# Kernel optimization log

Measured on AMD Instinct MI355X. Metric: run time of the kernel, lower is better.

Reference implementation:

```python
import jax, jax.numpy as jnp
import numpy as np

H, DH = 16, 64          # num_heads, dim_head
DIM = 1024              # dim_ltn
EPS = 1e-5


def setup_inputs() -> dict:
    key = jax.random.key(0)
    ks = jax.random.split(key, 8)
    b, n_txt, t, m = 2, 2048, 4, 256
    text = jax.random.normal(ks[0], (b, n_txt, DIM), dtype=jnp.float32)
    image = jax.random.normal(ks[1], (b, t, m, DIM), dtype=jnp.float32)
    locations = jax.random.randint(ks[2], (b, n_txt), 0, 2)  # 0/1 media markers
    s = DIM ** -0.5
    Wq = jax.random.normal(ks[3], (DIM, H * DH), dtype=jnp.float32) * s
    Wkv = jax.random.normal(ks[4], (DIM, 2 * H * DH), dtype=jnp.float32) * s
    Wo = jax.random.normal(ks[5], (H * DH, DIM), dtype=jnp.float32) * s
    ln_gamma = jnp.ones((DIM,), dtype=jnp.float32)
    ln_beta = jnp.zeros((DIM,), dtype=jnp.float32)
    return {"text": text, "image": image, "locations": locations,
            "Wq": Wq, "Wkv": Wkv, "Wo": Wo,
            "ln_gamma": ln_gamma, "ln_beta": ln_beta}


def reference(text, image, locations, Wq, Wkv, Wo, ln_gamma, ln_beta):
    scale = DH ** -0.5
    b, t, m, d = image.shape
    # LayerNorm(text)
    mu = text.mean(-1, keepdims=True)
    var = ((text - mu) ** 2).mean(-1, keepdims=True)
    tn = (text - mu) / jnp.sqrt(var + EPS) * ln_gamma + ln_beta
    img = image.reshape(b, t * m, d)             # b (t m) d
    q = tn @ Wq                                  # b n (h dh)
    k, v = jnp.split(img @ Wkv, 2, axis=-1)      # each b tm (h dh)
    split_heads = lambda x: x.reshape(x.shape[0], x.shape[1], H, DH).transpose(0, 2, 1, 3)
    q, k, v = split_heads(q), split_heads(k), split_heads(v)
    attn = jnp.einsum('bhid,bhjd->bhij', q, k) * scale   # b h n (t m)
    txt_time = jnp.cumsum(locations, axis=-1)            # b n : media index per text token
    viz_time = jnp.repeat(jnp.arange(1, t + 1), m)       # (t m)
    # only_attend_to_immediate -> equality mask
    mask = txt_time[:, None, :, None] == viz_time[None, None, None, :]
    neg = -jnp.finfo(attn.dtype).max
    attn = jnp.where(mask, attn, neg)
    attn = jax.nn.softmax(attn, axis=-1)
    # zero attention for text tokens before any media (txt_time == 0)
    attn = jnp.where((txt_time == 0)[:, None, :, None], 0.0, attn)
    out = jnp.einsum('bhij,bhjd->bhid', attn, v)
    out = out.transpose(0, 2, 1, 3).reshape(b, -1, H * DH)
    return out @ Wo
```

## Files before the change

### kernel.cpp

```cpp
#include <hip/hip_runtime.h>

#define BATCH 2
#define NTXT  2048
#define TMED  4
#define MMED  256
#define TM    (TMED * MMED)
#define DIM   1024
#define NH    16
#define DHD   64
#define KVW   2048
#define RMAX  256
#define RT    32
#define QSTR  ((size_t)BATCH * RMAX * DIM)

typedef _Float16 f16x8 __attribute__((ext_vector_type(8)));
typedef float    f32x4 __attribute__((ext_vector_type(4)));

__global__ __launch_bounds__(1024) void k1_scan_ibar(
    const int* __restrict__ loc, const float* __restrict__ image,
    int* __restrict__ tt, int* __restrict__ seg, float* __restrict__ ibar) {
  __shared__ int buf[NTXT];
  __shared__ int s_start, s_end;
  const int idx = blockIdx.x;
  const int tid = threadIdx.x;
  if (idx < BATCH) {
    const int b = idx;
    if (tid == 0) { s_start = NTXT; s_end = NTXT; }
    buf[tid]        = loc[b * NTXT + tid];
    buf[tid + 1024] = loc[b * NTXT + tid + 1024];
    __syncthreads();
    for (int off = 1; off < NTXT; off <<= 1) {
      int a0 = (tid >= off) ? buf[tid - off] : 0;
      int a1 = buf[tid + 1024 - off];
      __syncthreads();
      buf[tid] += a0;
      buf[tid + 1024] += a1;
      __syncthreads();
    }
    const int v0 = buf[tid], v1 = buf[tid + 1024];
    tt[b * NTXT + tid]        = v0;
    tt[b * NTXT + tid + 1024] = v1;
    if (v0 >= 1) atomicMin(&s_start, tid);
    if (v0 >= 5) atomicMin(&s_end, tid);
    if (v1 >= 1) atomicMin(&s_start, tid + 1024);
    if (v1 >= 5) atomicMin(&s_end, tid + 1024);
    __syncthreads();
    if (tid == 0) {
      seg[b * 2]     = s_start;
      seg[b * 2 + 1] = s_end - s_start;
    }
  } else {
    const int j = idx - BATCH;
    const int b = j >> 6, rt = j & 63;
    const float* p = image + (size_t)(b * TM + rt * 16) * DIM + tid;
    float s = 0.f;
#pragma unroll
    for (int r = 0; r < 16; r++) s += p[(size_t)r * DIM];
    atomicAdd(&ibar[b * DIM + tid], s * (1.0f / (float)TM));
  }
}

__global__ __launch_bounds__(256) void k2_prep(
    const float* __restrict__ Wkv, const float* __restrict__ text,
    const float* __restrict__ gamma, const float* __restrict__ beta,
    const int* __restrict__ seg, const float* __restrict__ ibar,
    _Float16* __restrict__ WkvT, float* __restrict__ tn,
    float* __restrict__ vbar) {
  __shared__ float tile[64][65];
  __shared__ float red[256];
  const int idx = blockIdx.x;
  const int tid = threadIdx.x;
  if (idx < 512) {
    const int k0 = (idx & 15) * 64, n0 = (idx >> 4) * 64;
    const int r = tid >> 4, c4 = (tid & 15) * 4;
#pragma unroll
    for (int i = 0; i < 4; i++) {
      const float4 v = *reinterpret_cast<const float4*>(
          Wkv + (size_t)(k0 + r + i * 16) * KVW + n0 + c4);
      tile[r + i * 16][c4 + 0] = v.x; tile[r + i * 16][c4 + 1] = v.y;
      tile[r + i * 16][c4 + 2] = v.z; tile[r + i * 16][c4 + 3] = v.w;
    }
    __syncthreads();
#pragma unroll
    for (int it = 0; it < 2; it++) {
      const int chunk = it * 256 + tid;
      const int n = chunk >> 3, kc = (chunk & 7) * 8;
      f16x8 h;
#pragma unroll
      for (int j = 0; j < 8; j++) h[j] = (_Float16)tile[kc + j][n];
      *reinterpret_cast<f16x8*>(WkvT + (size_t)(n0 + n) * DIM + k0 + kc) = h;
    }
  } else if (idx < 576) {
    const int j = idx - 512;
    const int b = j >> 5, rt = j & 31;
    const int i0 = seg[b * 2];
    const int cnt = min(seg[b * 2 + 1], RMAX);
    for (int r = rt; r < cnt; r += RT) {
      const float* xrow = text + (size_t)(b * NTXT + i0 + r) * DIM;
      float x[4];
      float s = 0.f;
#pragma unroll
      for (int u = 0; u < 4; u++) { x[u] = xrow[tid + 256 * u]; s += x[u]; }
      red[tid] = s; __syncthreads();
      for (int st = 128; st > 0; st >>= 1) {
        if (tid < st) red[tid] += red[tid + st];
        __syncthreads();
      }
      const float mu = red[0] * (1.0f / DIM); __syncthreads();
      float vs = 0.f;
#pragma unroll
      for (int u = 0; u < 4; u++) { float d = x[u] - mu; vs += d * d; }
      red[tid] = vs; __syncthreads();
      for (int st = 128; st > 0; st >>= 1) {
        if (tid < st) red[tid] += red[tid + st];
        __syncthreads();
      }
      const float rstd = rsqrtf(red[0] * (1.0f / DIM) + 1e-5f); __syncthreads();
      float* trow = tn + (size_t)(b * RMAX + r) * DIM;
#pragma unroll
      for (int u = 0; u < 4; u++) {
        const int c = tid + 256 * u;
        trow[c] = (x[u] - mu) * rstd * gamma[c] + beta[c];
      }
      __syncthreads();
    }
  } else {
    const int j = idx - 576;
    const int b = j >> 5, et = (j >> 3) & 3, cc = j & 7;
    const int e = et * 256 + tid;
    const int c0 = cc * 128;
    if (tid < 128) red[tid] = ibar[b * DIM + c0 + tid];
    __syncthreads();
    float s = 0.f;
    for (int c = 0; c < 128; c++)
      s += red[c] * Wkv[(size_t)(c0 + c) * KVW + DIM + e];
    atomicAdd(&vbar[b * DIM + e], s);
  }
}

__global__ __launch_bounds__(512) void k3_gemm_qproj_obar(
    const float* __restrict__ image, const _Float16* __restrict__ WkvT,
    const float* __restrict__ Wq, const float* __restrict__ Wo,
    const float* __restrict__ tn, const float* __restrict__ vbar,
    const int* __restrict__ seg, _Float16* __restrict__ kv16,
    float* __restrict__ qpart, float* __restrict__ obar) {
  __shared__ char smem[24576];
  const int idx = blockIdx.x;
  const int tid = threadIdx.x;
  if (idx < 256) {
    _Float16* As = (_Float16*)smem;
    _Float16* Bs = As + 128 * 32;
    const int lane = tid & 63, wid = tid >> 6;
    const int wm = wid & 3, wn = wid >> 2;
    const int row0 = (idx >> 4) * 128, col0 = (idx & 15) * 128;
    const int srow = tid >> 2, skc = (tid & 3) * 8;
    const int frow = lane & 15, fq = lane >> 4;
    f32x4 acc[2][4] = {};
    for (int k0 = 0; k0 < DIM; k0 += 32) {
      const float* ap = image + (size_t)(row0 + srow) * DIM + k0 + skc;
      const float4 a0 = *reinterpret_cast<const float4*>(ap);
      const float4 a1 = *reinterpret_cast<const float4*>(ap + 4);
      f16x8 av;
      av[0] = (_Float16)a0.x; av[1] = (_Float16)a0.y;
      av[2] = (_Float16)a0.z; av[3] = (_Float16)a0.w;
      av[4] = (_Float16)a1.x; av[5] = (_Float16)a1.y;
      av[6] = (_Float16)a1.z; av[7] = (_Float16)a1.w;
      const f16x8 bv = *reinterpret_cast<const f16x8*>(
          WkvT + (size_t)(col0 + srow) * DIM + k0 + skc);
      __syncthreads();
      *reinterpret_cast<f16x8*>(As + tid * 8) = av;
      *reinterpret_cast<f16x8*>(Bs + tid * 8) = bv;
      __syncthreads();
      f16x8 af[2], bf[4];
#pragma unroll
      for (int mt = 0; mt < 2; mt++)
        af[mt] = *reinterpret_cast<const f16x8*>(
            As + (wm * 32 + mt * 16 + frow) * 32 + fq * 8);
#pragma unroll
      for (int nt = 0; nt < 4; nt++)
        bf[nt] = *reinterpret_cast<const f16x8*>(
            Bs + (wn * 64 + nt * 16 + frow) * 32 + fq * 8);
#pragma unroll
      for (int mt = 0; mt < 2; mt++)
#pragma unroll
        for (int nt = 0; nt < 4; nt++)
          acc[mt][nt] = __builtin_amdgcn_mfma_f32_16x16x32_f16(
              af[mt], bf[nt], acc[mt][nt], 0, 0, 0);
    }
#pragma unroll
    for (int mt = 0; mt < 2; mt++)
#pragma unroll
      for (int nt = 0; nt < 4; nt++) {
        const int col = col0 + wn * 64 + nt * 16 + frow;
#pragma unroll
        for (int r = 0; r < 4; r++) {
          const int row = row0 + wm * 32 + mt * 16 + fq * 4 + r;
          kv16[(size_t)row * KVW + col] = (_Float16)acc[mt][nt][r];
        }
      }
  } else if (idx < 320) {
    float* tn_s = (float*)smem;
    float* qred = tn_s + 8 * 256;
    const int j = idx - 256;
    const int b = j >> 5, nt = (j >> 2) & 7, cc = j & 3;
    const int n0 = nt * 128, c0 = cc * 256;
    const int n = tid & 127, cs = tid >> 7;
    const int cnt = min(seg[b * 2 + 1], RMAX);
    float* qp = qpart + (size_t)cc * QSTR;
    for (int r0 = 0; r0 < cnt; r0 += 8) {
      const int rows = min(8, cnt - r0);
      for (int i = tid; i < 8 * 256; i += 512) {
        const int r = i >> 8, c = i & 255;
        tn_s[i] = (r < rows) ? tn[(size_t)(b * RMAX + r0 + r) * DIM + c0 + c]
                             : 0.f;
      }
      __syncthreads();
      float acc[8] = {};
      for (int ci = 0; ci < 64; ci++) {
        const int c = cs * 64 + ci;
        const float w = Wq[(size_t)(c0 + c) * DIM + n0 + n];
#pragma unroll
        for (int rr = 0; rr < 8; rr++) acc[rr] += tn_s[rr * 256 + c] * w;
      }
#pragma unroll
      for (int rr = 0; rr < 8; rr++) qred[(cs * 8 + rr) * 128 + n] = acc[rr];
      __syncthreads();
      if (cs == 0) {
        for (int rr = 0; rr < rows; rr++) {
          const float s = qred[rr * 128 + n] + qred[(8 + rr) * 128 + n] +
                          qred[(16 + rr) * 128 + n] + qred[(24 + rr) * 128 + n];
          qp[(size_t)(b * RMAX + r0 + rr) * DIM + n0 + n] = s;
        }
      }
      __syncthreads();
    }
  } else {
    float* vb_s = (float*)smem;
    const int j = idx - 320;
    const int b = j >> 4, et = (j >> 3) & 1, cc = j & 7;
    const int e = et * 512 + tid;
    const int c0 = cc * 128;
    if (tid < 128) vb_s[tid] = vbar[b * DIM + c0 + tid];
    __syncthreads();
    float s = 0.f;
    for (int c = 0; c < 128; c++)
      s += vb_s[c] * Wo[(size_t)(c0 + c) * DIM + e];
    atomicAdd(&obar[b * DIM + e], s);
  }
}

__global__ __launch_bounds__(256) void k4_fill_attn(
    const float* __restrict__ text, const _Float16* __restrict__ kv16,
    const float* __restrict__ Wq, const float* __restrict__ Wo,
    const float* __restrict__ gamma, const float* __restrict__ beta,
    const int* __restrict__ tt, const int* __restrict__ seg,
    const float* __restrict__ obar, const float* __restrict__ qpart,
    float* __restrict__ oacc, float* __restrict__ out) {
  __shared__ float red[256];
  __shared__ float pbuf[256];
  const int idx = blockIdx.x;
  const int tid = threadIdx.x;
  if (idx < BATCH * NTXT) {
    const int b = idx >> 11;
    const int i = idx & (NTXT - 1);
    const int t = tt[b * NTXT + i];
    float* orow = out + (size_t)(b * NTXT + i) * DIM;
    if (t == 0) {
      for (int c = tid; c < DIM; c += 256) orow[c] = 0.f;
      return;
    }
    if (t > TMED) {
      const float* ob = obar + b * DIM;
      for (int c = tid; c < DIM; c += 256) orow[c] = ob[c];
      return;
    }
    if (i - seg[b * 2] < RMAX) return;
    __shared__ float tns[DIM];
    __shared__ float qrow[DIM];
    __shared__ float oaccs[DIM];
    const float* xrow = text + (size_t)(b * NTXT + i) * DIM;
    float x[4];
    float s = 0.f;
#pragma unroll
    for (int u = 0; u < 4; u++) { x[u] = xrow[tid + 256 * u]; s += x[u]; }
    red[tid] = s; __syncthreads();
    for (int st = 128; st > 0; st >>= 1) {
      if (tid < st) red[tid] += red[tid + st];
      __syncthreads();
    }
    const float mu = red[0] * (1.0f / DIM); __syncthreads();
    float vs = 0.f;
#pragma unroll
    for (int u = 0; u < 4; u++) { float d = x[u] - mu; vs += d * d; }
    red[tid] = vs; __syncthreads();
    for (int st = 128; st > 0; st >>= 1) {
      if (tid < st) red[tid] += red[tid + st];
      __syncthreads();
    }
    const float rstd = rsqrtf(red[0] * (1.0f / DIM) + 1e-5f); __syncthreads();
#pragma unroll
    for (int u = 0; u < 4; u++) {
      const int c = tid + 256 * u;
      tns[c] = (x[u] - mu) * rstd * gamma[c] + beta[c];
    }
    __syncthreads();
    {
      float qa[4] = {0.f, 0.f, 0.f, 0.f};
      for (int c = 0; c < DIM; c++) {
        const float tv = tns[c];
        const float* w = Wq + (size_t)c * DIM + tid;
#pragma unroll
        for (int u = 0; u < 4; u++) qa[u] += tv * w[256 * u];
      }
#pragma unroll
      for (int u = 0; u < 4; u++) qrow[tid + 256 * u] = qa[u];
    }
    __syncthreads();
    const size_t kvrow0 = (size_t)(b * TM + (t - 1) * MMED) * KVW;
    const int d0 = tid & 63, g = tid >> 6;
    for (int h = 0; h < NH; h++) {
      const _Float16* krow = kv16 + kvrow0 + (size_t)tid * KVW + h * DHD;
      float sc = 0.f;
#pragma unroll
      for (int d = 0; d < DHD; d++) sc += qrow[h * DHD + d] * (float)krow[d];
      sc *= 0.125f;
      red[tid] = sc; __syncthreads();
      for (int st = 128; st > 0; st >>= 1) {
        if (tid < st) red[tid] = fmaxf(red[tid], red[tid + st]);
        __syncthreads();
      }
      const float mx = red[0]; __syncthreads();
      const float e = __expf(sc - mx);
      red[tid] = e; __syncthreads();
      for (int st = 128; st > 0; st >>= 1) {
        if (tid < st) red[tid] += red[tid + st];
        __syncthreads();
      }
      const float inv = 1.0f / red[0]; __syncthreads();
      pbuf[tid] = e * inv; __syncthreads();
      const _Float16* vbase = kv16 + kvrow0 + (size_t)(g * 64) * KVW + DIM + h * DHD + d0;
      float a = 0.f;
#pragma unroll 8
      for (int jj = 0; jj < 64; jj++) a += pbuf[g * 64 + jj] * (float)vbase[(size_t)jj * KVW];
      red[tid] = a; __syncthreads();
      if (tid < 64)
        oaccs[h * DHD + tid] = red[tid] + red[64 + tid] + red[128 + tid] + red[192 + tid];
      __syncthreads();
    }
    float oa[4] = {0.f, 0.f, 0.f, 0.f};
    for (int c = 0; c < DIM; c++) {
      const float ov = oaccs[c];
      const float* w = Wo + (size_t)c * DIM + tid;
#pragma unroll
      for (int u = 0; u < 4; u++) oa[u] += ov * w[256 * u];
    }
#pragma unroll
    for (int u = 0; u < 4; u++) orow[tid + 256 * u] = oa[u];
  } else {
    __shared__ float qs[DHD];
    const int j = idx - BATCH * NTXT;
    const int h = j & 15, rt = (j >> 4) & 31, b = j >> 9;
    const int i0 = seg[b * 2];
    const int cnt = min(seg[b * 2 + 1], RMAX);
    const int d0 = tid & 63, g = tid >> 6;
    for (int r = rt; r < cnt; r += RT) {
      const int i = i0 + r;
      const int t = tt[b * NTXT + i];
      if (tid < 64) {
        const size_t qoff = (size_t)(b * RMAX + r) * DIM + h * DHD + tid;
        qs[tid] = qpart[qoff] + qpart[QSTR + qoff] +
                  qpart[2 * QSTR + qoff] + qpart[3 * QSTR + qoff];
      }
      __syncthreads();
      const size_t kvrow0 = (size_t)(b * TM + (t - 1) * MMED) * KVW;
      const _Float16* krow = kv16 + kvrow0 + (size_t)tid * KVW + h * DHD;
      float sc = 0.f;
#pragma unroll
      for (int d = 0; d < DHD; d += 8) {
        const f16x8 kk = *reinterpret_cast<const f16x8*>(krow + d);
#pragma unroll
        for (int u = 0; u < 8; u++) sc += qs[d + u] * (float)kk[u];
      }
      sc *= 0.125f;
      red[tid] = sc; __syncthreads();
      for (int st = 128; st > 0; st >>= 1) {
        if (tid < st) red[tid] = fmaxf(red[tid], red[tid + st]);
        __syncthreads();
      }
      const float mx = red[0]; __syncthreads();
      const float e = __expf(sc - mx);
      red[tid] = e; __syncthreads();
      for (int st = 128; st > 0; st >>= 1) {
        if (tid < st) red[tid] += red[tid + st];
        __syncthreads();
      }
      const float inv = 1.0f / red[0]; __syncthreads();
      pbuf[tid] = e * inv; __syncthreads();
      const _Float16* vbase = kv16 + kvrow0 + (size_t)(g * 64) * KVW + DIM + h * DHD + d0;
      float a = 0.f;
#pragma unroll 8
      for (int jj = 0; jj < 64; jj++) a += pbuf[g * 64 + jj] * (float)vbase[(size_t)jj * KVW];
      red[tid] = a; __syncthreads();
      if (tid < 64)
        oacc[(size_t)(b * RMAX + r) * DIM + h * DHD + tid] =
            red[tid] + red[64 + tid] + red[128 + tid] + red[192 + tid];
      __syncthreads();
    }
  }
}

__global__ __launch_bounds__(256) void k5_oproj(
    const float* __restrict__ oacc, const float* __restrict__ Wo,
    const int* __restrict__ seg, float* __restrict__ out) {
  const int ct = blockIdx.x;
  const int rt = blockIdx.y;
  const int b = blockIdx.z;
  const int i0 = seg[b * 2];
  const int cnt = min(seg[b * 2 + 1], RMAX);
  const int tid = threadIdx.x;
  const int d0 = tid & 63, g = tid >> 6;
  __shared__ float op[4][64];
  for (int r = rt; r < cnt; r += RT) {
    const float* arow = oacc + (size_t)(b * RMAX + r) * DIM;
    const float* wo = Wo + (size_t)(g * 256) * DIM + ct * 64 + d0;
    float s = 0.f;
    for (int c = 0; c < 256; c++) s += arow[g * 256 + c] * wo[(size_t)c * DIM];
    op[g][d0] = s; __syncthreads();
    if (tid < 64)
      out[(size_t)(b * NTXT + i0 + r) * DIM + ct * 64 + tid] =
          op[0][tid] + op[1][tid] + op[2][tid] + op[3][tid];
    __syncthreads();
  }
}

extern "C" void kernel_launch(void* const* d_in, const int* in_sizes, int n_in,
                              void* d_out, int out_size, void* d_ws, size_t ws_size,
                              hipStream_t stream) {
  const float* text  = (const float*)d_in[0];
  const float* image = (const float*)d_in[1];
  const int*   loc   = (const int*)d_in[2];
  const float* Wq    = (const float*)d_in[3];
  const float* Wkv   = (const float*)d_in[4];
  const float* Wo    = (const float*)d_in[5];
  const float* gamma = (const float*)d_in[6];
  const float* beta  = (const float*)d_in[7];
  float* out = (float*)d_out;

  _Float16* kv16  = (_Float16*)d_ws;
  _Float16* WkvT  = kv16 + (size_t)BATCH * TM * KVW;
  float*    oacc  = (float*)WkvT;
  float*    tn    = (float*)(WkvT + (size_t)KVW * DIM);
  float*    qpart = tn + (size_t)BATCH * RMAX * DIM;
  float*    ibar  = qpart + 4 * QSTR;
  float*    vbar  = ibar + BATCH * DIM;
  float*    obar  = vbar + BATCH * DIM;
  int*      tt    = (int*)(obar + BATCH * DIM);
  int*      seg   = tt + BATCH * NTXT;

  hipMemsetAsync(ibar, 0, 3 * BATCH * DIM * sizeof(float), stream);
  k1_scan_ibar<<<BATCH + 128, 1024, 0, stream>>>(loc, image, tt, seg, ibar);
  k2_prep<<<640, 256, 0, stream>>>(Wkv, text, gamma, beta, seg, ibar,
                                   WkvT, tn, vbar);
  k3_gemm_qproj_obar<<<352, 512, 0, stream>>>(image, WkvT, Wq, Wo, tn, vbar,
                                              seg, kv16, qpart, obar);
  k4_fill_attn<<<BATCH * NTXT + NH * RT * BATCH, 256, 0, stream>>>(
      text, kv16, Wq, Wo, gamma, beta, tt, seg, obar, qpart, oacc, out);
  k5_oproj<<<dim3(16, RT, BATCH), 256, 0, stream>>>(oacc, Wo, seg, out);
}
```

Baseline: 166.3 us.

## Restructure pipeline: fuse LN into q-proj, vbar from GEMM epilogue, fold o-proj into attention

Removes the separate image-mean pass and ibar·Wkv GEMV. vbar is now computed by reducing the V columns of the KV GEMM accumulators in its epilogue. LayerNorm moves into the q-projection blocks using warp-shuffle single-pass statistics, and the prefix scan becomes a per-thread serial scan plus a block scan. The o-projection kernel is dropped: each attention head block multiplies its head output by its slice of Wo and atomically adds into pre-zeroed output rows. This cuts launches and global intermediates, at the cost of many float atomics, nondeterministic summation order and a single-pass variance formula.

```diff
diff --git a/kernel.cpp b/kernel.cpp
--- a/kernel.cpp
+++ b/kernel.cpp
@@ -10,67 +10,53 @@
 #define DHD   64
 #define KVW   2048
 #define RMAX  256
-#define RT    32
 #define QSTR  ((size_t)BATCH * RMAX * DIM)
 
 typedef _Float16 f16x8 __attribute__((ext_vector_type(8)));
 typedef float    f32x4 __attribute__((ext_vector_type(4)));
 
-__global__ __launch_bounds__(1024) void k1_scan_ibar(
-    const int* __restrict__ loc, const float* __restrict__ image,
-    int* __restrict__ tt, int* __restrict__ seg, float* __restrict__ ibar) {
-  __shared__ int buf[NTXT];
+__global__ __launch_bounds__(256) void k1_prep(
+    const int* __restrict__ loc, const float* __restrict__ Wkv,
+    int* __restrict__ tt, int* __restrict__ seg, float* __restrict__ vbar,
+    _Float16* __restrict__ WkvT) {
+  __shared__ float tile[64][65];
+  __shared__ int tots[256];
   __shared__ int s_start, s_end;
-  const int idx = blockIdx.x;
+  const int bid = blockIdx.x;
   const int tid = threadIdx.x;
-  if (idx < BATCH) {
-    const int b = idx;
+  if (bid < BATCH) {
+    const int b = bid;
     if (tid == 0) { s_start = NTXT; s_end = NTXT; }
-    buf[tid]        = loc[b * NTXT + tid];
-    buf[tid + 1024] = loc[b * NTXT + tid + 1024];
-    __syncthreads();
-    for (int off = 1; off < NTXT; off <<= 1) {
-      int a0 = (tid >= off) ? buf[tid - off] : 0;
-      int a1 = buf[tid + 1024 - off];
-      __syncthreads();
-      buf[tid] += a0;
-      buf[tid + 1024] += a1;
-      __syncthreads();
-    }
-    const int v0 = buf[tid], v1 = buf[tid + 1024];
-    tt[b * NTXT + tid]        = v0;
-    tt[b * NTXT + tid + 1024] = v1;
-    if (v0 >= 1) atomicMin(&s_start, tid);
-    if (v0 >= 5) atomicMin(&s_end, tid);
-    if (v1 >= 1) atomicMin(&s_start, tid + 1024);
-    if (v1 >= 5) atomicMin(&s_end, tid + 1024);
+    __syncthreads();
+    int v[8];
+    int run = 0;
+    const int base = b * NTXT + tid * 8;
+#pragma unroll
+    for (int k = 0; k < 8; k++) { run += loc[base + k]; v[k] = run; }
+    tots[tid] = run; __syncthreads();
+    for (int off = 1; off < 256; off <<= 1) {
+      const int add = (tid >= off) ? tots[tid - off] : 0;
+      __syncthreads();
+      tots[tid] += add;
+      __syncthreads();
+    }
+    const int excl = tots[tid] - run;
+#pragma unroll
+    for (int k = 0; k < 8; k++) {
+      const int tv = excl + v[k];
+      tt[base + k] = tv;
+      if (tv >= 1) atomicMin(&s_start, tid * 8 + k);
+      if (tv >= 5) atomicMin(&s_end, tid * 8 + k);
+    }
     __syncthreads();
     if (tid == 0) {
       seg[b * 2]     = s_start;
       seg[b * 2 + 1] = s_end - s_start;
     }
+  } else if (bid == 2) {
+    for (int c = tid; c < 2 * BATCH * DIM; c += 256) vbar[c] = 0.f;
   } else {
-    const int j = idx - BATCH;
-    const int b = j >> 6, rt = j & 63;
-    const float* p = image + (size_t)(b * TM + rt * 16) * DIM + tid;
-    float s = 0.f;
-#pragma unroll
-    for (int r = 0; r < 16; r++) s += p[(size_t)r * DIM];
-    atomicAdd(&ibar[b * DIM + tid], s * (1.0f / (float)TM));
-  }
-}
-
-__global__ __launch_bounds__(256) void k2_prep(
-    const float* __restrict__ Wkv, const float* __restrict__ text,
-    const float* __restrict__ gamma, const float* __restrict__ beta,
-    const int* __restrict__ seg, const float* __restrict__ ibar,
-    _Float16* __restrict__ WkvT, float* __restrict__ tn,
-    float* __restrict__ vbar) {
-  __shared__ float tile[64][65];
-  __shared__ float red[256];
-  const int idx = blockIdx.x;
-  const int tid = threadIdx.x;
-  if (idx < 512) {
+    const int idx = bid - 3;
     const int k0 = (idx & 15) * 64, n0 = (idx >> 4) * 64;
     const int r = tid >> 4, c4 = (tid & 15) * 4;
 #pragma unroll
@@ -90,61 +76,16 @@
       for (int j = 0; j < 8; j++) h[j] = (_Float16)tile[kc + j][n];
       *reinterpret_cast<f16x8*>(WkvT + (size_t)(n0 + n) * DIM + k0 + kc) = h;
     }
-  } else if (idx < 576) {
-    const int j = idx - 512;
-    const int b = j >> 5, rt = j & 31;
-    const int i0 = seg[b * 2];
-    const int cnt = min(seg[b * 2 + 1], RMAX);
-    for (int r = rt; r < cnt; r += RT) {
-      const float* xrow = text + (size_t)(b * NTXT + i0 + r) * DIM;
-      float x[4];
-      float s = 0.f;
-#pragma unroll
-      for (int u = 0; u < 4; u++) { x[u] = xrow[tid + 256 * u]; s += x[u]; }
-      red[tid] = s; __syncthreads();
-      for (int st = 128; st > 0; st >>= 1) {
-        if (tid < st) red[tid] += red[tid + st];
-        __syncthreads();
-      }
-      const float mu = red[0] * (1.0f / DIM); __syncthreads();
-      float vs = 0.f;
-#pragma unroll
-      for (int u = 0; u < 4; u++) { float d = x[u] - mu; vs += d * d; }
-      red[tid] = vs; __syncthreads();
-      for (int st = 128; st > 0; st >>= 1) {
-        if (tid < st) red[tid] += red[tid + st];
-        __syncthreads();
-      }
-      const float rstd = rsqrtf(red[0] * (1.0f / DIM) + 1e-5f); __syncthreads();
-      float* trow = tn + (size_t)(b * RMAX + r) * DIM;
-#pragma unroll
-      for (int u = 0; u < 4; u++) {
-        const int c = tid + 256 * u;
-        trow[c] = (x[u] - mu) * rstd * gamma[c] + beta[c];
-      }
-      __syncthreads();
-    }
-  } else {
-    const int j = idx - 576;
-    const int b = j >> 5, et = (j >> 3) & 3, cc = j & 7;
-    const int e = et * 256 + tid;
-    const int c0 = cc * 128;
-    if (tid < 128) red[tid] = ibar[b * DIM + c0 + tid];
-    __syncthreads();
-    float s = 0.f;
-    for (int c = 0; c < 128; c++)
-      s += red[c] * Wkv[(size_t)(c0 + c) * KVW + DIM + e];
-    atomicAdd(&vbar[b * DIM + e], s);
   }
 }
 
-__global__ __launch_bounds__(512) void k3_gemm_qproj_obar(
+__global__ __launch_bounds__(512) void k2_gemm_qproj(
     const float* __restrict__ image, const _Float16* __restrict__ WkvT,
-    const float* __restrict__ Wq, const float* __restrict__ Wo,
-    const float* __restrict__ tn, const float* __restrict__ vbar,
+    const float* __restrict__ text, const float* __restrict__ Wq,
+    const float* __restrict__ gamma, const float* __restrict__ beta,
     const int* __restrict__ seg, _Float16* __restrict__ kv16,
-    float* __restrict__ qpart, float* __restrict__ obar) {
-  __shared__ char smem[24576];
+    float* __restrict__ qpart, float* __restrict__ vbar) {
+  __shared__ char smem[16384];
   const int idx = blockIdx.x;
   const int tid = threadIdx.x;
   if (idx < 256) {
@@ -198,54 +139,97 @@
           kv16[(size_t)row * KVW + col] = (_Float16)acc[mt][nt][r];
         }
       }
-  } else if (idx < 320) {
+    if (col0 >= DIM) {
+      const int b = row0 >> 10;
+#pragma unroll
+      for (int nt = 0; nt < 4; nt++) {
+        float s = 0.f;
+#pragma unroll
+        for (int mt = 0; mt < 2; mt++)
+#pragma unroll
+          for (int r = 0; r < 4; r++) s += acc[mt][nt][r];
+        s += __shfl_down(s, 32);
+        s += __shfl_down(s, 16);
+        if (lane < 16)
+          atomicAdd(&vbar[b * DIM + (col0 - DIM) + wn * 64 + nt * 16 + lane],
+                    s * (1.0f / (float)TM));
+      }
+    }
+  } else {
     float* tn_s = (float*)smem;
-    float* qred = tn_s + 8 * 256;
     const int j = idx - 256;
     const int b = j >> 5, nt = (j >> 2) & 7, cc = j & 3;
     const int n0 = nt * 128, c0 = cc * 256;
-    const int n = tid & 127, cs = tid >> 7;
+    const int lane = tid & 63, w = tid >> 6;
+    const int n = tid & 127, rp = tid >> 7;
+    const int i0 = seg[b * 2];
     const int cnt = min(seg[b * 2 + 1], RMAX);
     float* qp = qpart + (size_t)cc * QSTR;
     for (int r0 = 0; r0 < cnt; r0 += 8) {
       const int rows = min(8, cnt - r0);
-      for (int i = tid; i < 8 * 256; i += 512) {
-        const int r = i >> 8, c = i & 255;
-        tn_s[i] = (r < rows) ? tn[(size_t)(b * RMAX + r0 + r) * DIM + c0 + c]
-                             : 0.f;
-      }
-      __syncthreads();
-      float acc[8] = {};
-      for (int ci = 0; ci < 64; ci++) {
-        const int c = cs * 64 + ci;
-        const float w = Wq[(size_t)(c0 + c) * DIM + n0 + n];
-#pragma unroll
-        for (int rr = 0; rr < 8; rr++) acc[rr] += tn_s[rr * 256 + c] * w;
-      }
-#pragma unroll
-      for (int rr = 0; rr < 8; rr++) qred[(cs * 8 + rr) * 128 + n] = acc[rr];
-      __syncthreads();
-      if (cs == 0) {
-        for (int rr = 0; rr < rows; rr++) {
-          const float s = qred[rr * 128 + n] + qred[(8 + rr) * 128 + n] +
-                          qred[(16 + rr) * 128 + n] + qred[(24 + rr) * 128 + n];
-          qp[(size_t)(b * RMAX + r0 + rr) * DIM + n0 + n] = s;
+      if (w < rows) {
+        const float* xrow = text + (size_t)(b * NTXT + i0 + r0 + w) * DIM;
+        float s = 0.f, sq = 0.f;
+#pragma unroll
+        for (int u = 0; u < 16; u++) {
+          const float x = xrow[lane + 64 * u];
+          s += x; sq += x * x;
         }
-      }
-      __syncthreads();
-    }
-  } else {
-    float* vb_s = (float*)smem;
-    const int j = idx - 320;
-    const int b = j >> 4, et = (j >> 3) & 1, cc = j & 7;
-    const int e = et * 512 + tid;
-    const int c0 = cc * 128;
+#pragma unroll
+        for (int off = 32; off > 0; off >>= 1) {
+          s += __shfl_xor(s, off);
+          sq += __shfl_xor(sq, off);
+        }
+        const float mu = s * (1.0f / DIM);
+        const float rstd = rsqrtf(sq * (1.0f / DIM) - mu * mu + 1e-5f);
+#pragma unroll
+        for (int u = 0; u < 4; u++) {
+          const int c = c0 + lane + 64 * u;
+          tn_s[w * 256 + lane + 64 * u] =
+              (xrow[c] - mu) * rstd * gamma[c] + beta[c];
+        }
+      }
+      __syncthreads();
+      float a0 = 0.f, a1 = 0.f;
+      for (int c = 0; c < 256; c++) {
+        const float wv = Wq[(size_t)(c0 + c) * DIM + n0 + n];
+        a0 += tn_s[(rp * 2) * 256 + c] * wv;
+        a1 += tn_s[(rp * 2 + 1) * 256 + c] * wv;
+      }
+      if (rp * 2 < rows)
+        qp[(size_t)(b * RMAX + r0 + rp * 2) * DIM + n0 + n] = a0;
+      if (rp * 2 + 1 < rows)
+        qp[(size_t)(b * RMAX + r0 + rp * 2 + 1) * DIM + n0 + n] = a1;
+      __syncthreads();
+    }
+  }
+}
+
+__global__ __launch_bounds__(512) void k3_obar_zero(
+    const float* __restrict__ vbar, const float* __restrict__ Wo,
+    const int* __restrict__ seg, float* __restrict__ obar,
+    float* __restrict__ out) {
+  __shared__ float vb_s[128];
+  const int bid = blockIdx.x;
+  const int tid = threadIdx.x;
+  if (bid < 32) {
+    const int b = bid >> 4, et = (bid >> 3) & 1, cc = bid & 7;
+    const int e = et * 512 + tid, c0 = cc * 128;
     if (tid < 128) vb_s[tid] = vbar[b * DIM + c0 + tid];
     __syncthreads();
     float s = 0.f;
     for (int c = 0; c < 128; c++)
       s += vb_s[c] * Wo[(size_t)(c0 + c) * DIM + e];
     atomicAdd(&obar[b * DIM + e], s);
+  } else {
+    const int b = bid - 32;
+    const int i0 = seg[b * 2];
+    const int cnt = min(seg[b * 2 + 1], RMAX);
+    for (int r = 0; r < cnt; r++) {
+      float* orow = out + (size_t)(b * NTXT + i0 + r) * DIM;
+      orow[tid] = 0.f;
+      orow[tid + 512] = 0.f;
+    }
   }
 }
 
@@ -255,7 +239,7 @@
     const float* __restrict__ gamma, const float* __restrict__ beta,
     const int* __restrict__ tt, const int* __restrict__ seg,
     const float* __restrict__ obar, const float* __restrict__ qpart,
-    float* __restrict__ oacc, float* __restrict__ out) {
+    float* __restrict__ out) {
   __shared__ float red[256];
   __shared__ float pbuf[256];
   const int idx = blockIdx.x;
@@ -263,22 +247,23 @@
   if (idx < BATCH * NTXT) {
     const int b = idx >> 11;
     const int i = idx & (NTXT - 1);
-    const int t = tt[b * NTXT + i];
-    float* orow = out + (size_t)(b * NTXT + i) * DIM;
+    const int t = tt[idx];
+    float* orow = out + (size_t)idx * DIM;
     if (t == 0) {
-      for (int c = tid; c < DIM; c += 256) orow[c] = 0.f;
+      *reinterpret_cast<float4*>(&orow[tid * 4]) =
+          make_float4(0.f, 0.f, 0.f, 0.f);
       return;
     }
     if (t > TMED) {
-      const float* ob = obar + b * DIM;
-      for (int c = tid; c < DIM; c += 256) orow[c] = ob[c];
+      *reinterpret_cast<float4*>(&orow[tid * 4]) =
+          *reinterpret_cast<const float4*>(&obar[b * DIM + tid * 4]);
       return;
     }
     if (i - seg[b * 2] < RMAX) return;
     __shared__ float tns[DIM];
     __shared__ float qrow[DIM];
     __shared__ float oaccs[DIM];
-    const float* xrow = text + (size_t)(b * NTXT + i) * DIM;
+    const float* xrow = text + (size_t)idx * DIM;
     float x[4];
     float s = 0.f;
 #pragma unroll
@@ -308,9 +293,9 @@
       float qa[4] = {0.f, 0.f, 0.f, 0.f};
       for (int c = 0; c < DIM; c++) {
         const float tv = tns[c];
-        const float* w = Wq + (size_t)c * DIM + tid;
-#pragma unroll
-        for (int u = 0; u < 4; u++) qa[u] += tv * w[256 * u];
+        const float* wp = Wq + (size_t)c * DIM + tid;
+#pragma unroll
+        for (int u = 0; u < 4; u++) qa[u] += tv * wp[256 * u];
       }
 #pragma unroll
       for (int u = 0; u < 4; u++) qrow[tid + 256 * u] = qa[u];
@@ -338,32 +323,36 @@
       }
       const float inv = 1.0f / red[0]; __syncthreads();
       pbuf[tid] = e * inv; __syncthreads();
-      const _Float16* vbase = kv16 + kvrow0 + (size_t)(g * 64) * KVW + DIM + h * DHD + d0;
+      const _Float16* vbase =
+          kv16 + kvrow0 + (size_t)(g * 64) * KVW + DIM + h * DHD + d0;
       float a = 0.f;
 #pragma unroll 8
-      for (int jj = 0; jj < 64; jj++) a += pbuf[g * 64 + jj] * (float)vbase[(size_t)jj * KVW];
+      for (int jj = 0; jj < 64; jj++)
+        a += pbuf[g * 64 + jj] * (float)vbase[(size_t)jj * KVW];
       red[tid] = a; __syncthreads();
       if (tid < 64)
-        oaccs[h * DHD + tid] = red[tid] + red[64 + tid] + red[128 + tid] + red[192 + tid];
+        oaccs[h * DHD + tid] =
+            red[tid] + red[64 + tid] + red[128 + tid] + red[192 + tid];
       __syncthreads();
     }
     float oa[4] = {0.f, 0.f, 0.f, 0.f};
     for (int c = 0; c < DIM; c++) {
       const float ov = oaccs[c];
-      const float* w = Wo + (size_t)c * DIM + tid;
-#pragma unroll
-      for (int u = 0; u < 4; u++) oa[u] += ov * w[256 * u];
+      const float* wp = Wo + (size_t)c * DIM + tid;
+#pragma unroll
+      for (int u = 0; u < 4; u++) oa[u] += ov * wp[256 * u];
     }
 #pragma unroll
     for (int u = 0; u < 4; u++) orow[tid + 256 * u] = oa[u];
   } else {
     __shared__ float qs[DHD];
+    __shared__ float oacc_s[DHD];
     const int j = idx - BATCH * NTXT;
     const int h = j & 15, rt = (j >> 4) & 31, b = j >> 9;
     const int i0 = seg[b * 2];
     const int cnt = min(seg[b * 2 + 1], RMAX);
     const int d0 = tid & 63, g = tid >> 6;
-    for (int r = rt; r < cnt; r += RT) {
+    for (int r = rt; r < cnt; r += 32) {
       const int i = i0 + r;
       const int t = tt[b * NTXT + i];
       if (tid < 64) {
@@ -396,40 +385,28 @@
       }
       const float inv = 1.0f / red[0]; __syncthreads();
       pbuf[tid] = e * inv; __syncthreads();
-      const _Float16* vbase = kv16 + kvrow0 + (size_t)(g * 64) * KVW + DIM + h * DHD + d0;
+      const _Float16* vbase =
+          kv16 + kvrow0 + (size_t)(g * 64) * KVW + DIM + h * DHD + d0;
       float a = 0.f;
 #pragma unroll 8
-      for (int jj = 0; jj < 64; jj++) a += pbuf[g * 64 + jj] * (float)vbase[(size_t)jj * KVW];
+      for (int jj = 0; jj < 64; jj++)
+        a += pbuf[g * 64 + jj] * (float)vbase[(size_t)jj * KVW];
       red[tid] = a; __syncthreads();
       if (tid < 64)
-        oacc[(size_t)(b * RMAX + r) * DIM + h * DHD + tid] =
-            red[tid] + red[64 + tid] + red[128 + tid] + red[192 + tid];
-      __syncthreads();
-    }
-  }
-}
-
-__global__ __launch_bounds__(256) void k5_oproj(
-    const float* __restrict__ oacc, const float* __restrict__ Wo,
-    const int* __restrict__ seg, float* __restrict__ out) {
-  const int ct = blockIdx.x;
-  const int rt = blockIdx.y;
-  const int b = blockIdx.z;
-  const int i0 = seg[b * 2];
-  const int cnt = min(seg[b * 2 + 1], RMAX);
-  const int tid = threadIdx.x;
-  const int d0 = tid & 63, g = tid >> 6;
-  __shared__ float op[4][64];
-  for (int r = rt; r < cnt; r += RT) {
-    const float* arow = oacc + (size_t)(b * RMAX + r) * DIM;
-    const float* wo = Wo + (size_t)(g * 256) * DIM + ct * 64 + d0;
-    float s = 0.f;
-    for (int c = 0; c < 256; c++) s += arow[g * 256 + c] * wo[(size_t)c * DIM];
-    op[g][d0] = s; __syncthreads();
-    if (tid < 64)
-      out[(size_t)(b * NTXT + i0 + r) * DIM + ct * 64 + tid] =
-          op[0][tid] + op[1][tid] + op[2][tid] + op[3][tid];
-    __syncthreads();
+        oacc_s[tid] = red[tid] + red[64 + tid] + red[128 + tid] + red[192 + tid];
+      __syncthreads();
+      float* orow = out + (size_t)(b * NTXT + i) * DIM;
+#pragma unroll
+      for (int u = 0; u < 4; u++) {
+        const int e2 = tid + 256 * u;
+        float s2 = 0.f;
+#pragma unroll 8
+        for (int d = 0; d < DHD; d++)
+          s2 += oacc_s[d] * Wo[(size_t)(h * DHD + d) * DIM + e2];
+        atomicAdd(&orow[e2], s2);
+      }
+      __syncthreads();
+    }
   }
 }
 
@@ -448,22 +425,16 @@
 
   _Float16* kv16  = (_Float16*)d_ws;
   _Float16* WkvT  = kv16 + (size_t)BATCH * TM * KVW;
-  float*    oacc  = (float*)WkvT;
-  float*    tn    = (float*)(WkvT + (size_t)KVW * DIM);
-  float*    qpart = tn + (size_t)BATCH * RMAX * DIM;
-  float*    ibar  = qpart + 4 * QSTR;
-  float*    vbar  = ibar + BATCH * DIM;
+  float*    qpart = (float*)(WkvT + (size_t)KVW * DIM);
+  float*    vbar  = qpart + 4 * QSTR;
   float*    obar  = vbar + BATCH * DIM;
   int*      tt    = (int*)(obar + BATCH * DIM);
   int*      seg   = tt + BATCH * NTXT;
 
-  hipMemsetAsync(ibar, 0, 3 * BATCH * DIM * sizeof(float), stream);
-  k1_scan_ibar<<<BATCH + 128, 1024, 0, stream>>>(loc, image, tt, seg, ibar);
-  k2_prep<<<640, 256, 0, stream>>>(Wkv, text, gamma, beta, seg, ibar,
-                                   WkvT, tn, vbar);
-  k3_gemm_qproj_obar<<<352, 512, 0, stream>>>(image, WkvT, Wq, Wo, tn, vbar,
-                                              seg, kv16, qpart, obar);
-  k4_fill_attn<<<BATCH * NTXT + NH * RT * BATCH, 256, 0, stream>>>(
-      text, kv16, Wq, Wo, gamma, beta, tt, seg, obar, qpart, oacc, out);
-  k5_oproj<<<dim3(16, RT, BATCH), 256, 0, stream>>>(oacc, Wo, seg, out);
+  k1_prep<<<515, 256, 0, stream>>>(loc, Wkv, tt, seg, vbar, WkvT);
+  k2_gemm_qproj<<<320, 512, 0, stream>>>(image, WkvT, text, Wq, gamma, beta,
+                                         seg, kv16, qpart, vbar);
+  k3_obar_zero<<<34, 512, 0, stream>>>(vbar, Wo, seg, obar, out);
+  k4_fill_attn<<<BATCH * NTXT + NH * 32 * BATCH, 256, 0, stream>>>(
+      text, kv16, Wq, Wo, gamma, beta, tt, seg, obar, qpart, out);
 }
```

Result: slower. 182.4 us (+9.7%).
